# Optimization experiments

Measured on AMD Instinct MI355X. Metric: run time of the kernel, lower is better.

The kernel has to match this reference:

```python
import jax, jax.numpy as jnp
import numpy as np

B, S, D, H = 4, 2048, 1024, 16
HD = D // H          # head_dim = 64; per-head scale = sqrt(HD) as in source
FF = 4096
EPS = 1e-5


def _layernorm(x, g, b):
    m = jnp.mean(x, axis=-1, keepdims=True)
    v = jnp.mean(jnp.square(x - m), axis=-1, keepdims=True)
    return (x - m) * jax.lax.rsqrt(v + EPS) * g + b


def setup_inputs() -> dict:
    key = jax.random.key(0)
    ks = jax.random.split(key, 10)
    std = 0.02
    return {
        "x": jax.random.normal(ks[0], (B, S, D), jnp.float32),
        "wq": jax.random.normal(ks[1], (H, D, HD), jnp.float32) * std,
        "bq": jnp.zeros((H, HD), jnp.float32),
        "wk": jax.random.normal(ks[2], (H, D, HD), jnp.float32) * std,
        "bk": jnp.zeros((H, HD), jnp.float32),
        "wv": jax.random.normal(ks[3], (H, D, HD), jnp.float32) * std,
        "bv": jnp.zeros((H, HD), jnp.float32),
        "wo": jax.random.normal(ks[4], (D, D), jnp.float32) * std,
        "bo": jnp.zeros((D,), jnp.float32),
        "w1": jax.random.normal(ks[5], (D, FF), jnp.float32) * std,
        "b1": jnp.zeros((FF,), jnp.float32),
        "w2": jax.random.normal(ks[6], (FF, D), jnp.float32) * std,
        "b2": jnp.zeros((D,), jnp.float32),
        "g1": jnp.ones((D,), jnp.float32),
        "beta1": jnp.zeros((D,), jnp.float32),
        "g2": jnp.ones((D,), jnp.float32),
        "beta2": jnp.zeros((D,), jnp.float32),
    }


def reference(x, wq, bq, wk, bk, wv, bv, wo, bo, w1, b1, w2, b2, g1, beta1, g2, beta2):
    # Per-head Q/K/V projections (stacked over heads) -> [B,H,S,HD]
    q = jnp.einsum('bsd,hdf->bhsf', x, wq) + bq[None, :, None, :]
    k = jnp.einsum('bsd,hdf->bhsf', x, wk) + bk[None, :, None, :]
    v = jnp.einsum('bsd,hdf->bhsf', x, wv) + bv[None, :, None, :]

    scale = jnp.sqrt(jnp.asarray(HD, jnp.float32))
    att = jnp.einsum('bhqf,bhkf->bhqk', q, k) / scale  # [B,H,S,S]
    causal = jnp.tril(jnp.ones((S, S), dtype=bool))
    att = jnp.where(causal[None, None], att, -jnp.inf)
    p = jax.nn.softmax(att, axis=-1)
    o = jnp.einsum('bhqk,bhkf->bhqf', p, v)            # [B,H,S,HD]
    o = o.transpose(0, 2, 1, 3).reshape(B, S, D)       # concat heads
    attn_out = o @ wo + bo

    h = _layernorm(x + attn_out, g1, beta1)            # post-LN, dropout=0 (eval)
    ff = jax.nn.gelu(h @ w1 + b1, approximate=False) @ w2 + b2
    return _layernorm(h + ff, g2, beta2)
```

## Files before the change

kernel.cpp:

```cpp
#include <hip/hip_runtime.h>
#include <hip/hip_bf16.h>
#include <math.h>

typedef __bf16 bf16x8 __attribute__((ext_vector_type(8)));
typedef float floatx4 __attribute__((ext_vector_type(4)));
typedef unsigned short ushort8 __attribute__((ext_vector_type(8)));
typedef unsigned short ushort4v __attribute__((ext_vector_type(4)));

__device__ __forceinline__ unsigned short f2bs(float f){
  union { float f; unsigned u; } v; v.f = f;
  unsigned r = v.u + 0x7fffu + ((v.u >> 16) & 1u);
  return (unsigned short)(r >> 16);
}
__device__ __forceinline__ float bs2f(unsigned short s){
  union { unsigned u; float f; } v; v.u = ((unsigned)s) << 16; return v.f;
}
__device__ __forceinline__ unsigned pk2(float a, float b){
  union { __hip_bfloat162 h; unsigned u; } cv;
  cv.h = __float22bfloat162_rn(make_float2(a, b));
  return cv.u;
}
__device__ __forceinline__ void gl_lds16(const void* g, void* l){
  __builtin_amdgcn_global_load_lds(
      (const __attribute__((address_space(1))) void*)g,
      (__attribute__((address_space(3))) void*)l,
      16, 0, 0);
}

__global__ __launch_bounds__(256) void cvt_x(const float* __restrict__ x,
                                             unsigned short* __restrict__ o){
  const int i = (blockIdx.x*256 + threadIdx.x)*4;
  const float4 v = *(const float4*)(x + i);
  ushort4v u = { f2bs(v.x), f2bs(v.y), f2bs(v.z), f2bs(v.w) };
  *(ushort4v*)(o + i) = u;
}

__global__ __launch_bounds__(256) void transpose_pack(const float* __restrict__ src,
                                                      unsigned short* __restrict__ dst,
                                                      int R, int C){
  __shared__ float tile[32][65];
  const int r0 = blockIdx.y*32, c0 = blockIdx.x*64;
  const int t = threadIdx.x;
  {
    const int r = t >> 3, cc = (t & 7)*8;
    const float* p = src + (size_t)(r0+r)*C + c0 + cc;
    const float4 v0 = *(const float4*)p;
    const float4 v1 = *(const float4*)(p+4);
    tile[r][cc+0]=v0.x; tile[r][cc+1]=v0.y; tile[r][cc+2]=v0.z; tile[r][cc+3]=v0.w;
    tile[r][cc+4]=v1.x; tile[r][cc+5]=v1.y; tile[r][cc+6]=v1.z; tile[r][cc+7]=v1.w;
  }
  __syncthreads();
  const int f = t >> 2, rr = (t & 3)*8;
  ushort8 u;
  #pragma unroll
  for (int j=0;j<8;j++) u[j] = f2bs(tile[rr+j][f]);
  *(ushort8*)(dst + (size_t)(c0+f)*R + r0 + rr) = u;
}

__global__ __launch_bounds__(256) void pack_qkv(const float* __restrict__ wq,
                                                const float* __restrict__ wk,
                                                const float* __restrict__ wv,
                                                const float* __restrict__ bq,
                                                const float* __restrict__ bk,
                                                const float* __restrict__ bv,
                                                unsigned short* __restrict__ Wt,
                                                float* __restrict__ Bc){
  __shared__ float tile[32][65];
  const int dt = blockIdx.x, h = blockIdx.y, sel = blockIdx.z;
  const float* src = (sel==0 ? wq : (sel==1 ? wk : wv)) + (size_t)h*65536;
  const int t = threadIdx.x, d0 = dt*32;
  {
    const int r = t >> 3, cc = (t & 7)*8;
    const float* p = src + (size_t)(d0+r)*64 + cc;
    const float4 v0 = *(const float4*)p;
    const float4 v1 = *(const float4*)(p+4);
    tile[r][cc+0]=v0.x; tile[r][cc+1]=v0.y; tile[r][cc+2]=v0.z; tile[r][cc+3]=v0.w;
    tile[r][cc+4]=v1.x; tile[r][cc+5]=v1.y; tile[r][cc+6]=v1.z; tile[r][cc+7]=v1.w;
  }
  __syncthreads();
  const int f = t >> 2, rr = (t & 3)*8;
  ushort8 u;
  #pragma unroll
  for (int j=0;j<8;j++) u[j] = f2bs(tile[rr+j][f]);
  const size_t n = (size_t)sel*1024 + h*64 + f;
  *(ushort8*)(Wt + n*1024 + d0 + rr) = u;
  if (dt==0 && t<64){
    const float* bs = (sel==0 ? bq : (sel==1 ? bk : bv)) + h*64;
    Bc[sel*1024 + h*64 + t] = bs[t];
  }
}

template<int MODE>
__global__ __launch_bounds__(256, 4)
void gemm_tn(const unsigned short* __restrict__ A,
             const unsigned short* __restrict__ Bt,
             const float* __restrict__ bias,
             void* __restrict__ out0,
             void* __restrict__ out1,
             void* __restrict__ out2,
             int K, int OW, int klen){
  __shared__ __align__(16) unsigned short As[128*32];
  __shared__ __align__(16) unsigned short Bs[128*32];
  const int tid = threadIdx.x;
  const int wave = tid >> 6, lane = tid & 63;
  const int quad = lane >> 4, l15 = lane & 15;
  const int lin = blockIdx.x;
  const int n0 = (lin & 63) << 7;
  const int m0 = (lin >> 6) << 7;
  const int kz = blockIdx.z;
  const int kbase = kz * klen;
  const int wr = (wave >> 1) << 6, wc = (wave & 1) << 6;

  floatx4 acc[4][4];
  #pragma unroll
  for (int i=0;i<4;i++)
    #pragma unroll
    for (int j=0;j<4;j++) acc[i][j] = (floatx4)0.0f;

  const unsigned short* gA[2];
  const unsigned short* gB[2];
  int lofs[2];
  #pragma unroll
  for (int r2=0;r2<2;r2++){
    const int slot = r2*256 + tid;
    const int rp = slot >> 3, rem = slot & 7;
    const int row = rp*2 + (rem >> 2);
    const int kc = (rem & 3) ^ (rp & 3);
    gA[r2] = A  + (size_t)(m0 + row)*K + kbase + kc*8;
    gB[r2] = Bt + (size_t)(n0 + row)*K + kbase + kc*8;
    lofs[r2] = slot*8;
  }
  int aofs[4], bofs[4];
  #pragma unroll
  for (int t=0;t<4;t++){
    const int ra = wr + t*16 + l15;
    aofs[t] = (ra>>1)*64 + (ra&1)*32 + ((quad ^ ((ra>>1)&3))<<3);
    const int rb = wc + t*16 + l15;
    bofs[t] = (rb>>1)*64 + (rb&1)*32 + ((quad ^ ((rb>>1)&3))<<3);
  }

  for (int k0 = 0; k0 < klen; k0 += 32){
    gl_lds16(gA[0] + k0, As + lofs[0]);
    gl_lds16(gA[1] + k0, As + lofs[1]);
    gl_lds16(gB[0] + k0, Bs + lofs[0]);
    gl_lds16(gB[1] + k0, Bs + lofs[1]);
    __syncthreads();
    bf16x8 af[4];
    #pragma unroll
    for (int t=0;t<4;t++) af[t] = *(const bf16x8*)(&As[aofs[t]]);
    #pragma unroll
    for (int j=0;j<4;j++){
      const bf16x8 bv = *(const bf16x8*)(&Bs[bofs[j]]);
      #pragma unroll
      for (int i=0;i<4;i++)
        acc[i][j] = __builtin_amdgcn_mfma_f32_16x16x32_bf16(af[i], bv, acc[i][j], 0,0,0);
    }
    __syncthreads();
  }

  #pragma unroll
  for (int i=0;i<4;i++){
    const int row0 = m0 + wr + i*16 + quad*4;
    float4 b4 = make_float4(0.f,0.f,0.f,0.f);
    if (MODE != 4 || kz == 0) b4 = *(const float4*)(bias + row0);
    #pragma unroll
    for (int j=0;j<4;j++){
      const int tok = n0 + wc + j*16 + l15;
      float v0 = acc[i][j][0] + b4.x;
      float v1 = acc[i][j][1] + b4.y;
      float v2 = acc[i][j][2] + b4.z;
      float v3 = acc[i][j][3] + b4.w;
      if (MODE == 1){
        float4 o4; o4.x=v0; o4.y=v1; o4.z=v2; o4.w=v3;
        *(float4*)((float*)out0 + (size_t)tok*OW + row0) = o4;
      } else if (MODE == 2){
        float vv[4] = {v0,v1,v2,v3};
        #pragma unroll
        for (int r=0;r<4;r++){
          const float v = vv[r];
          const float u = 0.7978845608f*v*(1.0f + 0.044715f*v*v);
          const float e = __builtin_amdgcn_exp2f(u * 2.885390082f);
          vv[r] = 0.5f*v*(1.0f + (1.0f - 2.0f/(1.0f + e)));
        }
        uint2 pkd = make_uint2(pk2(vv[0], vv[1]), pk2(vv[2], vv[3]));
        *(uint2*)((unsigned short*)out0 + (size_t)tok*4096 + row0) = pkd;
      } else if (MODE == 4){
        uint2 pkd = make_uint2(pk2(v0, v1), pk2(v2, v3));
        unsigned short* o = (unsigned short*)(kz ? out1 : out0);
        *(uint2*)(o + (size_t)tok*1024 + row0) = pkd;
      } else {
        if (row0 < 1024){
          const float s = 0.18033688011112042f;
          uint2 pkd = make_uint2(pk2(v0*s, v1*s), pk2(v2*s, v3*s));
          *(uint2*)((unsigned short*)out0 + (size_t)tok*1024 + row0) = pkd;
        } else if (row0 < 2048){
          uint2 pkd = make_uint2(pk2(v0, v1), pk2(v2, v3));
          *(uint2*)((unsigned short*)out1 + (size_t)tok*1024 + (row0-1024)) = pkd;
        } else {
          uint2 pkd = make_uint2(pk2(v0, v1), pk2(v2, v3));
          *(uint2*)((unsigned short*)out2 + (size_t)tok*1024 + (row0-2048)) = pkd;
        }
      }
    }
  }
}

#define VMCNT4 asm volatile("s_waitcnt vmcnt(4)" ::: "memory")
#define VMCNT0 asm volatile("s_waitcnt vmcnt(0)" ::: "memory")
#define TAILW { if (tg < NT-2) VMCNT4; else VMCNT0; }
#define LGKM4 { asm volatile("s_waitcnt lgkmcnt(4)" ::: "memory"); __builtin_amdgcn_sched_barrier(0); }
#define LGKM8 { asm volatile("s_waitcnt lgkmcnt(8)" ::: "memory"); __builtin_amdgcn_sched_barrier(0); }
#define LGKM0 { asm volatile("s_waitcnt lgkmcnt(0)" ::: "memory"); __builtin_amdgcn_sched_barrier(0); }
#define PHASE_SYNC                                                            \
    __builtin_amdgcn_s_barrier();                                             \
    asm volatile("s_waitcnt lgkmcnt(0)" ::: "memory");                        \
    __builtin_amdgcn_sched_barrier(0);

#define STAGE_A(T, H) { const int T_ = (T); if (T_ < NT){                     \
    unsigned short* l_ = lds + (T_&1)*32768 + (H)*8192;                       \
    const int ko_ = kbase + (T_<<6);                                          \
    gl_lds16(srcA##H##_0 + ko_, l_ + ch0*8);                                  \
    gl_lds16(srcA##H##_1 + ko_, l_ + ch1*8); } }
#define STAGE_B(T, H) { const int T_ = (T); if (T_ < NT){                     \
    unsigned short* l_ = lds + (T_&1)*32768 + 16384 + (H)*8192;               \
    const int ko_ = kbase + (T_<<6);                                          \
    gl_lds16(srcB##H##_0 + ko_, l_ + ch0*8);                                  \
    gl_lds16(srcB##H##_1 + ko_, l_ + ch1*8); } }

#define MFMA_Q(AF, BF, MH, NH)                                                \
    __builtin_amdgcn_s_setprio(1);                                            \
    _Pragma("unroll")                                                         \
    for (int k_=0;k_<2;k_++)                                                  \
      _Pragma("unroll")                                                       \
      for (int m_=0;m_<4;m_++)                                                \
        _Pragma("unroll")                                                     \
        for (int n_=0;n_<2;n_++)                                              \
          acc[(MH)*4+m_][(NH)*2+n_] = __builtin_amdgcn_mfma_f32_16x16x32_bf16( \
              AF[m_][k_], BF[n_][k_], acc[(MH)*4+m_][(NH)*2+n_], 0,0,0);      \
    __builtin_amdgcn_s_setprio(0);

#define RD_A(DST, BASE)                                                       \
    _Pragma("unroll")                                                         \
    for (int m_=0;m_<4;m_++)                                                  \
      _Pragma("unroll")                                                       \
      for (int k_=0;k_<2;k_++) DST[m_][k_] = *(const bf16x8*)((BASE) + aoff[m_][k_]);
#define RD_B(DST, BASE)                                                       \
    _Pragma("unroll")                                                         \
    for (int n_=0;n_<2;n_++)                                                  \
      _Pragma("unroll")                                                       \
      for (int k_=0;k_<2;k_++) DST[n_][k_] = *(const bf16x8*)((BASE) + boff[n_][k_]);

template<int MODE, int PIPE>
__global__ __launch_bounds__(512, 2)
void gemm256(const unsigned short* __restrict__ A,
             const unsigned short* __restrict__ Bt,
             const float* __restrict__ bias,
             void* __restrict__ out0,
             void* __restrict__ out1,
             void* __restrict__ out2,
             int K, int klen){
  __shared__ __align__(16) unsigned short lds[65536];
  const int tid = threadIdx.x;
  const int wave = tid >> 6, lane = tid & 63;
  const int quad = lane >> 4, l15 = lane & 15;
  const int wm = wave >> 2, wn = wave & 3;
  const int lin = blockIdx.x;
  const int n0 = (lin & 31) << 8;
  const int m0 = (lin >> 5) << 8;
  const int kz = blockIdx.z;
  const int kbase = kz * klen;
  const int NT = klen >> 6;

  const int r0 = tid >> 3;
  const int r1 = r0 + 64;
  const int g0 = (tid & 7) ^ (r0 & 7);
  const int ch0 = tid, ch1 = tid + 512;

  const unsigned short* srcA0_0 = A  + (size_t)(m0 +       r0)*K + g0*8;
  const unsigned short* srcA0_1 = A  + (size_t)(m0 +       r1)*K + g0*8;
  const unsigned short* srcA1_0 = A  + (size_t)(m0 + 128 + r0)*K + g0*8;
  const unsigned short* srcA1_1 = A  + (size_t)(m0 + 128 + r1)*K + g0*8;
  const unsigned short* srcB0_0 = Bt + (size_t)(n0 +       r0)*K + g0*8;
  const unsigned short* srcB0_1 = Bt + (size_t)(n0 +       r1)*K + g0*8;
  const unsigned short* srcB1_0 = Bt + (size_t)(n0 + 128 + r0)*K + g0*8;
  const unsigned short* srcB1_1 = Bt + (size_t)(n0 + 128 + r1)*K + g0*8;

  const int xr = l15 & 7;
  int aoff[4][2], boff[2][2];
  #pragma unroll
  for (int m=0;m<4;m++){
    const int rh = wm*64 + m*16 + l15;
    #pragma unroll
    for (int k=0;k<2;k++)
      aoff[m][k] = rh*64 + (((k*4 + quad) ^ xr) << 3);
  }
  #pragma unroll
  for (int n=0;n<2;n++){
    const int rb = wn*32 + n*16 + l15;
    #pragma unroll
    for (int k=0;k<2;k++)
      boff[n][k] = rb*64 + (((k*4 + quad) ^ xr) << 3);
  }

  floatx4 acc[8][4];
  #pragma unroll
  for (int i=0;i<8;i++)
    #pragma unroll
    for (int j=0;j<4;j++) acc[i][j] = (floatx4)0.0f;

  bf16x8 af0[4][2], af1[4][2], bf0[2][2], bf1[2][2];

  STAGE_B(0,0); STAGE_A(0,0); STAGE_A(0,1); STAGE_B(0,1);
  STAGE_B(1,0); STAGE_A(1,0);
  VMCNT4;
  __builtin_amdgcn_s_barrier();

  if (PIPE == 0){
    for (int tg = 0; tg < NT; ++tg){
      const int d = tg & 1;
      const unsigned short* A0b = lds + d*32768;
      const unsigned short* A1b = A0b + 8192;
      const unsigned short* B0b = lds + d*32768 + 16384;
      const unsigned short* B1b = B0b + 8192;

      RD_A(af0, A0b);
      RD_B(bf0, B0b);
      STAGE_A(tg+1, 1);
      PHASE_SYNC;
      MFMA_Q(af0, bf0, 0, 0);
      __builtin_amdgcn_s_barrier();

      RD_B(bf1, B1b);
      STAGE_B(tg+1, 1);
      PHASE_SYNC;
      MFMA_Q(af0, bf1, 0, 1);
      __builtin_amdgcn_s_barrier();

      RD_A(af1, A1b);
      STAGE_B(tg+2, 0);
      PHASE_SYNC;
      MFMA_Q(af1, bf1, 1, 1);
      __builtin_amdgcn_s_barrier();

      STAGE_A(tg+2, 0);
      PHASE_SYNC;
      MFMA_Q(af1, bf0, 1, 0);
      TAILW;
      __builtin_amdgcn_s_barrier();
    }
  } else {
    RD_A(af0, lds);
    RD_B(bf0, lds + 16384);

    for (int tg = 0; tg < NT; ++tg){
      const int d = tg & 1;
      const unsigned short* A1b = lds + d*32768 + 8192;
      const unsigned short* B1b = lds + d*32768 + 16384 + 8192;

      RD_B(bf1, B1b);
      STAGE_A(tg+1, 1);
      LGKM4;
      MFMA_Q(af0, bf0, 0, 0);

      RD_A(af1, A1b);
      STAGE_B(tg+1, 1);
      LGKM8;
      MFMA_Q(af0, bf1, 0, 1);
      __builtin_amdgcn_s_barrier();

      STAGE_B(tg+2, 0);
      LGKM0;
      MFMA_Q(af1, bf1, 1, 1);

      STAGE_A(tg+2, 0);
      TAILW;
      __builtin_amdgcn_s_barrier();
      {
        const unsigned short* A0n = lds + (d^1)*32768;
        const unsigned short* B0n = A0n + 16384;
        if (tg+1 < NT){ RD_A(af0, A0n); }
        MFMA_Q(af1, bf0, 1, 0);
        if (tg+1 < NT){ RD_B(bf0, B0n); }
      }
    }
  }

  #pragma unroll
  for (int mh=0; mh<2; mh++){
    #pragma unroll
    for (int m=0; m<4; m++){
      const int row0 = m0 + mh*128 + wm*64 + m*16 + quad*4;
      float4 b4 = make_float4(0.f,0.f,0.f,0.f);
      if (MODE != 4 || kz == 0) b4 = *(const float4*)(bias + row0);
      #pragma unroll
      for (int nh=0; nh<2; nh++){
        #pragma unroll
        for (int n=0; n<2; n++){
          const int tok = n0 + nh*128 + wn*32 + n*16 + l15;
          const floatx4 a = acc[mh*4+m][nh*2+n];
          float v0 = a[0]+b4.x, v1 = a[1]+b4.y, v2 = a[2]+b4.z, v3 = a[3]+b4.w;
          if (MODE == 2){
            float vv[4] = {v0,v1,v2,v3};
            #pragma unroll
            for (int r=0;r<4;r++){
              const float v = vv[r];
              const float u = 0.7978845608f*v*(1.0f + 0.044715f*v*v);
              const float e = __builtin_amdgcn_exp2f(u * 2.885390082f);
              vv[r] = 0.5f*v*(1.0f + (1.0f - 2.0f/(1.0f + e)));
            }
            uint2 pkd = make_uint2(pk2(vv[0], vv[1]), pk2(vv[2], vv[3]));
            *(uint2*)((unsigned short*)out0 + (size_t)tok*4096 + row0) = pkd;
          } else if (MODE == 4){
            uint2 pkd = make_uint2(pk2(v0, v1), pk2(v2, v3));
            unsigned short* o = (unsigned short*)(kz ? out1 : out0);
            *(uint2*)(o + (size_t)tok*1024 + row0) = pkd;
          } else {
            if (row0 < 1024){
              const float s = 0.18033688011112042f;
              uint2 pkd = make_uint2(pk2(v0*s, v1*s), pk2(v2*s, v3*s));
              *(uint2*)((unsigned short*)out0 + (size_t)tok*1024 + row0) = pkd;
            } else if (row0 < 2048){
              uint2 pkd = make_uint2(pk2(v0, v1), pk2(v2, v3));
              *(uint2*)((unsigned short*)out1 + (size_t)tok*1024 + (row0-1024)) = pkd;
            } else {
              uint2 pkd = make_uint2(pk2(v0, v1), pk2(v2, v3));
              *(uint2*)((unsigned short*)out2 + (size_t)tok*1024 + (row0-2048)) = pkd;
            }
          }
        }
      }
    }
  }
}

__global__ __launch_bounds__(256) void vtrans(const unsigned short* __restrict__ Vtok,
                                              unsigned short* __restrict__ Vt){
  __shared__ unsigned short tile[64][65];
  const int st = blockIdx.x, bh = blockIdx.y;
  const int b = bh >> 4, h = bh & 15;
  const int t = threadIdx.x;
  {
    const int r = t >> 2, cc = (t & 3) * 16;
    const unsigned short* src = Vtok + (size_t)((b<<11) + (st<<6) + r)*1024 + (h<<6) + cc;
    ushort8 u0 = *(const ushort8*)src;
    ushort8 u1 = *(const ushort8*)(src + 8);
    #pragma unroll
    for (int j=0;j<8;j++){ tile[r][cc+j] = u0[j]; tile[r][cc+8+j] = u1[j]; }
  }
  __syncthreads();
  const int f = t >> 2, ss = (t & 3) * 16;
  ushort8 w0, w1;
  #pragma unroll
  for (int j=0;j<8;j++){ w0[j] = tile[ss+j][f]; w1[j] = tile[ss+8+j][f]; }
  unsigned short* dst = Vt + (size_t)bh*64*2048 + (size_t)f*2048 + (st<<6) + ss;
  *(ushort8*)dst = w0;
  *(ushort8*)(dst + 8) = w1;
}

__global__ __launch_bounds__(256, 4) void attn(const unsigned short* __restrict__ Q,
                                               const unsigned short* __restrict__ Kg,
                                               const unsigned short* __restrict__ Vt,
                                               unsigned short* __restrict__ O){
  __shared__ __align__(16) unsigned short Ks[64*64];
  __shared__ __align__(16) unsigned short Vs[64*64];
  __shared__ __align__(16) unsigned short PT[4][2][16*68];

  const int lin = blockIdx.x;
  const int bh = lin & 63;
  const int qt_lo = lin >> 6;
  const int qt_hi = 31 - qt_lo;
  const int b = bh >> 4, h = bh & 15;
  const int tid = threadIdx.x, wave = tid >> 6, lane = tid & 63;
  const int quad = lane >> 4, l15 = lane & 15;
  const float FM = 12.0f;

  const size_t qbase = (size_t)((b<<11) + (wave<<4) + l15)*1024 + (h<<6);
  bf16x8 qf_hi[2], qf_lo[2];
  qf_hi[0] = *(const bf16x8*)(Q + qbase + (size_t)(qt_hi<<6)*1024 + quad*8);
  qf_hi[1] = *(const bf16x8*)(Q + qbase + (size_t)(qt_hi<<6)*1024 + 32 + quad*8);
  qf_lo[0] = *(const bf16x8*)(Q + qbase + (size_t)(qt_lo<<6)*1024 + quad*8);
  qf_lo[1] = *(const bf16x8*)(Q + qbase + (size_t)(qt_lo<<6)*1024 + 32 + quad*8);

  floatx4 oa_hi[4], oa_lo[4];
  #pragma unroll
  for (int i=0;i<4;i++){ oa_hi[i] = (floatx4)0.0f; oa_lo[i] = (floatx4)0.0f; }
  float li_hi = 0.0f, li_lo = 0.0f;

  const unsigned short* Kbh = Kg + ((size_t)(b<<11))*1024 + (h<<6);
  const unsigned short* Vbh = Vt + (size_t)bh*64*2048;
  unsigned short* Pw0 = &PT[wave][0][0];
  unsigned short* Pw1 = &PT[wave][1][0];

  const int slot0 = wave*128 + lane;
  const int krow0 = slot0 >> 3, kc0 = (slot0 & 7) ^ (krow0 & 7);
  const int slot1 = slot0 + 64;
  const int krow1 = slot1 >> 3, kc1 = (slot1 & 7) ^ (krow1 & 7);

  auto softmax_P = [&](floatx4* sa, float& li, unsigned short* Pbuf, bool diag){
    if (diag){
      const int qrow = (wave<<4) + l15;
      #pragma unroll
      for (int tj=0;tj<4;tj++)
        #pragma unroll
        for (int r=0;r<4;r++)
          if (tj*16 + quad*4 + r > qrow) sa[tj][r] = -1e30f;
    }
    float rs = 0.0f;
    #pragma unroll
    for (int tj=0;tj<4;tj++)
      #pragma unroll
      for (int r=0;r<4;r++){
        const float p = __builtin_amdgcn_exp2f(sa[tj][r] - FM);
        sa[tj][r] = p;
        rs += p;
      }
    li += rs;
    #pragma unroll
    for (int tj=0;tj<4;tj++){
      uint2 pkd = make_uint2(pk2(sa[tj][0], sa[tj][1]), pk2(sa[tj][2], sa[tj][3]));
      *(uint2*)(Pbuf + l15*68 + tj*16 + quad*4) = pkd;
    }
  };

  for (int kt = 0; kt <= qt_hi; ++kt){
    gl_lds16(Kbh + (size_t)((kt<<6) + krow0)*1024 + kc0*8, Ks + wave*1024);
    gl_lds16(Kbh + (size_t)((kt<<6) + krow1)*1024 + kc1*8, Ks + wave*1024 + 512);
    gl_lds16(Vbh + (size_t)krow0*2048 + (kt<<6) + kc0*8, Vs + wave*1024);
    gl_lds16(Vbh + (size_t)krow1*2048 + (kt<<6) + kc1*8, Vs + wave*1024 + 512);
    __syncthreads();

    if (kt <= qt_lo){
      floatx4 sh[4], sl[4];
      __builtin_amdgcn_s_setprio(1);
      #pragma unroll
      for (int tj=0;tj<4;tj++){
        sh[tj] = (floatx4)0.0f; sl[tj] = (floatx4)0.0f;
        #pragma unroll
        for (int ks=0;ks<2;ks++){
          const int n = tj*16 + l15;
          const int c = (ks*4 + quad) ^ (n & 7);
          const bf16x8 kf = *(const bf16x8*)(Ks + n*64 + c*8);
          sh[tj] = __builtin_amdgcn_mfma_f32_16x16x32_bf16(kf, qf_hi[ks], sh[tj], 0,0,0);
          sl[tj] = __builtin_amdgcn_mfma_f32_16x16x32_bf16(kf, qf_lo[ks], sl[tj], 0,0,0);
        }
      }
      __builtin_amdgcn_s_setprio(0);
      softmax_P(sh, li_hi, Pw0, false);
      softmax_P(sl, li_lo, Pw1, kt == qt_lo);
      __builtin_amdgcn_s_setprio(1);
      #pragma unroll
      for (int ks2=0;ks2<2;ks2++){
        const bf16x8 pfh = *(const bf16x8*)(Pw0 + l15*68 + ks2*32 + quad*8);
        const bf16x8 pfl = *(const bf16x8*)(Pw1 + l15*68 + ks2*32 + quad*8);
        #pragma unroll
        for (int tn=0;tn<4;tn++){
          const int n2 = tn*16 + l15;
          const int c = (ks2*4 + quad) ^ (n2 & 7);
          const bf16x8 vf = *(const bf16x8*)(Vs + n2*64 + c*8);
          oa_hi[tn] = __builtin_amdgcn_mfma_f32_16x16x32_bf16(vf, pfh, oa_hi[tn], 0,0,0);
          oa_lo[tn] = __builtin_amdgcn_mfma_f32_16x16x32_bf16(vf, pfl, oa_lo[tn], 0,0,0);
        }
      }
      __builtin_amdgcn_s_setprio(0);
    } else {
      floatx4 sh[4];
      __builtin_amdgcn_s_setprio(1);
      #pragma unroll
      for (int tj=0;tj<4;tj++){
        sh[tj] = (floatx4)0.0f;
        #pragma unroll
        for (int ks=0;ks<2;ks++){
          const int n = tj*16 + l15;
          const int c = (ks*4 + quad) ^ (n & 7);
          const bf16x8 kf = *(const bf16x8*)(Ks + n*64 + c*8);
          sh[tj] = __builtin_amdgcn_mfma_f32_16x16x32_bf16(kf, qf_hi[ks], sh[tj], 0,0,0);
        }
      }
      __builtin_amdgcn_s_setprio(0);
      softmax_P(sh, li_hi, Pw0, kt == qt_hi);
      __builtin_amdgcn_s_setprio(1);
      #pragma unroll
      for (int ks2=0;ks2<2;ks2++){
        const bf16x8 pfh = *(const bf16x8*)(Pw0 + l15*68 + ks2*32 + quad*8);
        #pragma unroll
        for (int tn=0;tn<4;tn++){
          const int n2 = tn*16 + l15;
          const int c = (ks2*4 + quad) ^ (n2 & 7);
          const bf16x8 vf = *(const bf16x8*)(Vs + n2*64 + c*8);
          oa_hi[tn] = __builtin_amdgcn_mfma_f32_16x16x32_bf16(vf, pfh, oa_hi[tn], 0,0,0);
        }
      }
      __builtin_amdgcn_s_setprio(0);
    }
    __syncthreads();
  }

  li_hi += __shfl_xor(li_hi, 16, 64);
  li_hi += __shfl_xor(li_hi, 32, 64);
  li_lo += __shfl_xor(li_lo, 16, 64);
  li_lo += __shfl_xor(li_lo, 32, 64);
  {
    const float inv = 1.0f / li_hi;
    unsigned short* Orow = O + (size_t)((b<<11) + (qt_hi<<6) + (wave<<4) + l15)*1024 + (h<<6);
    #pragma unroll
    for (int tn=0;tn<4;tn++){
      uint2 pkd = make_uint2(pk2(oa_hi[tn][0]*inv, oa_hi[tn][1]*inv),
                             pk2(oa_hi[tn][2]*inv, oa_hi[tn][3]*inv));
      *(uint2*)(Orow + tn*16 + quad*4) = pkd;
    }
  }
  {
    const float inv = 1.0f / li_lo;
    unsigned short* Orow = O + (size_t)((b<<11) + (qt_lo<<6) + (wave<<4) + l15)*1024 + (h<<6);
    #pragma unroll
    for (int tn=0;tn<4;tn++){
      uint2 pkd = make_uint2(pk2(oa_lo[tn][0]*inv, oa_lo[tn][1]*inv),
                             pk2(oa_lo[tn][2]*inv, oa_lo[tn][3]*inv));
      *(uint2*)(Orow + tn*16 + quad*4) = pkd;
    }
  }
}

__global__ __launch_bounds__(256) void ln_res(const float* __restrict__ a,
                                              const float* __restrict__ bsrc,
                                              const float* __restrict__ g,
                                              const float* __restrict__ be,
                                              float* __restrict__ of,
                                              unsigned short* __restrict__ ob){
  __shared__ float red1[4], red2[4];
  const int row = blockIdx.x, t = threadIdx.x;
  const int wave = t >> 6, lane = t & 63;
  const float4 va = *(const float4*)(a + (size_t)row*1024 + t*4);
  const float4 vb = *(const float4*)(bsrc + (size_t)row*1024 + t*4);
  float xs[4] = {va.x+vb.x, va.y+vb.y, va.z+vb.z, va.w+vb.w};
  float s = xs[0]+xs[1]+xs[2]+xs[3];
  #pragma unroll
  for (int d=1; d<64; d<<=1) s += __shfl_xor(s, d, 64);
  if (lane==0) red1[wave] = s;
  __syncthreads();
  const float mean = (red1[0]+red1[1]+red1[2]+red1[3]) * (1.0f/1024.0f);
  float vsum = 0.0f;
  #pragma unroll
  for (int i=0;i<4;i++){ const float d = xs[i]-mean; vsum += d*d; }
  #pragma unroll
  for (int d=1; d<64; d<<=1) vsum += __shfl_xor(vsum, d, 64);
  if (lane==0) red2[wave] = vsum;
  __syncthreads();
  const float var = (red2[0]+red2[1]+red2[2]+red2[3]) * (1.0f/1024.0f);
  const float rs = rsqrtf(var + 1e-5f);
  const float4 gg = *(const float4*)(g + t*4);
  const float4 bb = *(const float4*)(be + t*4);
  float y[4];
  y[0] = (xs[0]-mean)*rs*gg.x + bb.x;
  y[1] = (xs[1]-mean)*rs*gg.y + bb.y;
  y[2] = (xs[2]-mean)*rs*gg.z + bb.z;
  y[3] = (xs[3]-mean)*rs*gg.w + bb.w;
  if (of){
    float4 o4; o4.x=y[0]; o4.y=y[1]; o4.z=y[2]; o4.w=y[3];
    *(float4*)(of + (size_t)row*1024 + t*4) = o4;
  }
  if (ob){
    ushort4v u = { f2bs(y[0]), f2bs(y[1]), f2bs(y[2]), f2bs(y[3]) };
    *(ushort4v*)(ob + (size_t)row*1024 + t*4) = u;
  }
}

__global__ __launch_bounds__(256) void ln_res2(const float* __restrict__ a,
                                               const unsigned short* __restrict__ p0,
                                               const unsigned short* __restrict__ p1,
                                               const float* __restrict__ g,
                                               const float* __restrict__ be,
                                               float* __restrict__ of){
  __shared__ float red1[4], red2[4];
  const int row = blockIdx.x, t = threadIdx.x;
  const int wave = t >> 6, lane = t & 63;
  const float4 va = *(const float4*)(a + (size_t)row*1024 + t*4);
  const ushort4v u0 = *(const ushort4v*)(p0 + (size_t)row*1024 + t*4);
  const ushort4v u1 = *(const ushort4v*)(p1 + (size_t)row*1024 + t*4);
  float xs[4] = { va.x + bs2f(u0[0]) + bs2f(u1[0]),
                  va.y + bs2f(u0[1]) + bs2f(u1[1]),
                  va.z + bs2f(u0[2]) + bs2f(u1[2]),
                  va.w + bs2f(u0[3]) + bs2f(u1[3]) };
  float s = xs[0]+xs[1]+xs[2]+xs[3];
  #pragma unroll
  for (int d=1; d<64; d<<=1) s += __shfl_xor(s, d, 64);
  if (lane==0) red1[wave] = s;
  __syncthreads();
  const float mean = (red1[0]+red1[1]+red1[2]+red1[3]) * (1.0f/1024.0f);
  float vsum = 0.0f;
  #pragma unroll
  for (int i=0;i<4;i++){ const float d = xs[i]-mean; vsum += d*d; }
  #pragma unroll
  for (int d=1; d<64; d<<=1) vsum += __shfl_xor(vsum, d, 64);
  if (lane==0) red2[wave] = vsum;
  __syncthreads();
  const float var = (red2[0]+red2[1]+red2[2]+red2[3]) * (1.0f/1024.0f);
  const float rs = rsqrtf(var + 1e-5f);
  const float4 gg = *(const float4*)(g + t*4);
  const float4 bb = *(const float4*)(be + t*4);
  float4 o4;
  o4.x = (xs[0]-mean)*rs*gg.x + bb.x;
  o4.y = (xs[1]-mean)*rs*gg.y + bb.y;
  o4.z = (xs[2]-mean)*rs*gg.z + bb.z;
  o4.w = (xs[3]-mean)*rs*gg.w + bb.w;
  *(float4*)(of + (size_t)row*1024 + t*4) = o4;
}

extern "C" void kernel_launch(void* const* d_in, const int* in_sizes, int n_in,
                              void* d_out, int out_size, void* d_ws, size_t ws_size,
                              hipStream_t stream){
  (void)in_sizes; (void)n_in; (void)out_size; (void)ws_size;
  const float* x  = (const float*)d_in[0];
  const float* wq = (const float*)d_in[1];
  const float* bq = (const float*)d_in[2];
  const float* wk = (const float*)d_in[3];
  const float* bk = (const float*)d_in[4];
  const float* wv = (const float*)d_in[5];
  const float* bv = (const float*)d_in[6];
  const float* wo = (const float*)d_in[7];
  const float* bo = (const float*)d_in[8];
  const float* w1 = (const float*)d_in[9];
  const float* b1 = (const float*)d_in[10];
  const float* w2 = (const float*)d_in[11];
  const float* b2 = (const float*)d_in[12];
  const float* g1 = (const float*)d_in[13];
  const float* be1= (const float*)d_in[14];
  const float* g2 = (const float*)d_in[15];
  const float* be2= (const float*)d_in[16];
  float* out = (float*)d_out;

  char* ws = (char*)d_ws;
  size_t off = 0;
  auto take = [&](size_t bytes)->char*{
    char* p = ws + off; off += (bytes + 255) & ~(size_t)255; return p;
  };
  unsigned short* Xb  = (unsigned short*)take(8192UL*1024*2);
  unsigned short* Qb  = (unsigned short*)take(8192UL*1024*2);
  unsigned short* Kb  = (unsigned short*)take(8192UL*1024*2);
  unsigned short* Vtb = (unsigned short*)take(8192UL*1024*2);
  unsigned short* Ob  = (unsigned short*)take(8192UL*1024*2);
  unsigned short* Midb= Qb;
  unsigned short* Vtok= (unsigned short*)take(8192UL*1024*2);
  unsigned short* Wqkv= (unsigned short*)take(3072UL*1024*2);
  float*          Bqkv= (float*)take(3072UL*4);
  unsigned short* Wot = (unsigned short*)take(1024UL*1024*2);
  unsigned short* W1t = (unsigned short*)take(4096UL*1024*2);
  unsigned short* W2t = (unsigned short*)take(1024UL*4096*2);
  float*          C1  = (float*)take(8192UL*1024*4);
  unsigned short* F0  = (unsigned short*)C1;
  unsigned short* F1  = F0 + 8192UL*1024;
  float*          Hf  = (float*)take(8192UL*1024*4);
  unsigned short* Hb  = (unsigned short*)take(8192UL*1024*2);

  cvt_x<<<8192, 256, 0, stream>>>(x, Xb);
  pack_qkv<<<dim3(32,16,3), 256, 0, stream>>>(wq, wk, wv, bq, bk, bv, Wqkv, Bqkv);
  transpose_pack<<<dim3(16,32),  256, 0, stream>>>(wo, Wot, 1024, 1024);
  transpose_pack<<<dim3(64,32),  256, 0, stream>>>(w1, W1t, 1024, 4096);
  transpose_pack<<<dim3(16,128), 256, 0, stream>>>(w2, W2t, 4096, 1024);

  gemm256<3,1><<<12*32, 512, 0, stream>>>(Wqkv, Xb, Bqkv, Qb, Kb, Vtok, 1024, 1024);
  vtrans<<<dim3(32,64), 256, 0, stream>>>(Vtok, Vtb);

  attn<<<1024, 256, 0, stream>>>(Qb, Kb, Vtb, Ob);

  gemm_tn<1><<<8*64, 256, 0, stream>>>(Wot, Ob, bo, C1, nullptr, nullptr, 1024, 1024, 1024);
  ln_res<<<8192, 256, 0, stream>>>(x, C1, g1, be1, Hf, Hb);

  gemm256<2,0><<<16*32, 512, 0, stream>>>(W1t, Hb, b1, Midb, nullptr, nullptr, 1024, 1024);
  gemm256<4,1><<<dim3(4*32,1,2), 512, 0, stream>>>(W2t, Midb, b2, F0, F1, nullptr, 4096, 2048);
  ln_res2<<<8192, 256, 0, stream>>>(Hf, F0, F1, g2, be2, out);
}
```

Before: 505.0 us.

## Fuse prep kernels into one launch and register-prefetch K/V tiles in attention

```diff
diff --git a/kernel.cpp b/kernel.cpp
--- a/kernel.cpp
+++ b/kernel.cpp
@@ -27,20 +27,58 @@
       16, 0, 0);
 }
 
-__global__ __launch_bounds__(256) void cvt_x(const float* __restrict__ x,
-                                             unsigned short* __restrict__ o){
-  const int i = (blockIdx.x*256 + threadIdx.x)*4;
-  const float4 v = *(const float4*)(x + i);
-  ushort4v u = { f2bs(v.x), f2bs(v.y), f2bs(v.z), f2bs(v.w) };
-  *(ushort4v*)(o + i) = u;
-}
-
-__global__ __launch_bounds__(256) void transpose_pack(const float* __restrict__ src,
-                                                      unsigned short* __restrict__ dst,
-                                                      int R, int C){
+__global__ __launch_bounds__(256) void prep(
+    const float* __restrict__ x,  unsigned short* __restrict__ Xb,
+    const float* __restrict__ wq, const float* __restrict__ wk,
+    const float* __restrict__ wv, const float* __restrict__ bq,
+    const float* __restrict__ bk, const float* __restrict__ bv,
+    unsigned short* __restrict__ Wqkv, float* __restrict__ Bqkv,
+    const float* __restrict__ wo, unsigned short* __restrict__ Wot,
+    const float* __restrict__ w1, unsigned short* __restrict__ W1t,
+    const float* __restrict__ w2, unsigned short* __restrict__ W2t){
   __shared__ float tile[32][65];
-  const int r0 = blockIdx.y*32, c0 = blockIdx.x*64;
-  const int t = threadIdx.x;
+  const int blk = blockIdx.x, t = threadIdx.x;
+
+  if (blk < 8192){
+    const int i = (blk*256 + t)*4;
+    const float4 v = *(const float4*)(x + i);
+    ushort4v u = { f2bs(v.x), f2bs(v.y), f2bs(v.z), f2bs(v.w) };
+    *(ushort4v*)(Xb + i) = u;
+    return;
+  }
+
+  if (blk < 9728){
+    const int p = blk - 8192;
+    const int dt = p & 31, h = (p>>5)&15, sel = p>>9;
+    const float* src = (sel==0 ? wq : (sel==1 ? wk : wv)) + (size_t)h*65536;
+    const int d0 = dt*32;
+    {
+      const int r = t >> 3, cc = (t & 7)*8;
+      const float* pp = src + (size_t)(d0+r)*64 + cc;
+      const float4 v0 = *(const float4*)pp;
+      const float4 v1 = *(const float4*)(pp+4);
+      tile[r][cc+0]=v0.x; tile[r][cc+1]=v0.y; tile[r][cc+2]=v0.z; tile[r][cc+3]=v0.w;
+      tile[r][cc+4]=v1.x; tile[r][cc+5]=v1.y; tile[r][cc+6]=v1.z; tile[r][cc+7]=v1.w;
+    }
+    __syncthreads();
+    const int f = t >> 2, rr = (t & 3)*8;
+    ushort8 u;
+    #pragma unroll
+    for (int j=0;j<8;j++) u[j] = f2bs(tile[rr+j][f]);
+    const size_t n = (size_t)sel*1024 + h*64 + f;
+    *(ushort8*)(Wqkv + n*1024 + d0 + rr) = u;
+    if (dt==0 && t<64){
+      const float* bs = (sel==0 ? bq : (sel==1 ? bk : bv)) + h*64;
+      Bqkv[sel*1024 + h*64 + t] = bs[t];
+    }
+    return;
+  }
+
+  const float* src; unsigned short* dst; int R, C, bx, by;
+  if (blk < 10240){ const int q = blk-9728;  src=wo; dst=Wot; R=1024; C=1024; bx=q&15; by=q>>4; }
+  else if (blk < 12288){ const int q = blk-10240; src=w1; dst=W1t; R=1024; C=4096; bx=q&63; by=q>>6; }
+  else { const int q = blk-12288; src=w2; dst=W2t; R=4096; C=1024; bx=q&15; by=q>>4; }
+  const int r0 = by*32, c0 = bx*64;
   {
     const int r = t >> 3, cc = (t & 7)*8;
     const float* p = src + (size_t)(r0+r)*C + c0 + cc;
@@ -55,39 +93,6 @@
   #pragma unroll
   for (int j=0;j<8;j++) u[j] = f2bs(tile[rr+j][f]);
   *(ushort8*)(dst + (size_t)(c0+f)*R + r0 + rr) = u;
-}
-
-__global__ __launch_bounds__(256) void pack_qkv(const float* __restrict__ wq,
-                                                const float* __restrict__ wk,
-                                                const float* __restrict__ wv,
-                                                const float* __restrict__ bq,
-                                                const float* __restrict__ bk,
-                                                const float* __restrict__ bv,
-                                                unsigned short* __restrict__ Wt,
-                                                float* __restrict__ Bc){
-  __shared__ float tile[32][65];
-  const int dt = blockIdx.x, h = blockIdx.y, sel = blockIdx.z;
-  const float* src = (sel==0 ? wq : (sel==1 ? wk : wv)) + (size_t)h*65536;
-  const int t = threadIdx.x, d0 = dt*32;
-  {
-    const int r = t >> 3, cc = (t & 7)*8;
-    const float* p = src + (size_t)(d0+r)*64 + cc;
-    const float4 v0 = *(const float4*)p;
-    const float4 v1 = *(const float4*)(p+4);
-    tile[r][cc+0]=v0.x; tile[r][cc+1]=v0.y; tile[r][cc+2]=v0.z; tile[r][cc+3]=v0.w;
-    tile[r][cc+4]=v1.x; tile[r][cc+5]=v1.y; tile[r][cc+6]=v1.z; tile[r][cc+7]=v1.w;
-  }
-  __syncthreads();
-  const int f = t >> 2, rr = (t & 3)*8;
-  ushort8 u;
-  #pragma unroll
-  for (int j=0;j<8;j++) u[j] = f2bs(tile[rr+j][f]);
-  const size_t n = (size_t)sel*1024 + h*64 + f;
-  *(ushort8*)(Wt + n*1024 + d0 + rr) = u;
-  if (dt==0 && t<64){
-    const float* bs = (sel==0 ? bq : (sel==1 ? bk : bv)) + h*64;
-    Bc[sel*1024 + h*64 + t] = bs[t];
-  }
 }
 
 template<int MODE>
@@ -496,6 +501,20 @@
   const int slot1 = slot0 + 64;
   const int krow1 = slot1 >> 3, kc1 = (slot1 & 7) ^ (krow1 & 7);
 
+  ushort8 kr0, kr1, vr0, vr1;
+  auto load_kv = [&](int kt){
+    kr0 = *(const ushort8*)(Kbh + (size_t)((kt<<6) + krow0)*1024 + kc0*8);
+    kr1 = *(const ushort8*)(Kbh + (size_t)((kt<<6) + krow1)*1024 + kc1*8);
+    vr0 = *(const ushort8*)(Vbh + (size_t)krow0*2048 + (kt<<6) + kc0*8);
+    vr1 = *(const ushort8*)(Vbh + (size_t)krow1*2048 + (kt<<6) + kc1*8);
+  };
+  auto write_kv = [&](){
+    *(ushort8*)(Ks + wave*1024 + lane*8)       = kr0;
+    *(ushort8*)(Ks + wave*1024 + 512 + lane*8) = kr1;
+    *(ushort8*)(Vs + wave*1024 + lane*8)       = vr0;
+    *(ushort8*)(Vs + wave*1024 + 512 + lane*8) = vr1;
+  };
+
   auto softmax_P = [&](floatx4* sa, float& li, unsigned short* Pbuf, bool diag){
     if (diag){
       const int qrow = (wave<<4) + l15;
@@ -522,12 +541,11 @@
     }
   };
 
+  load_kv(0); write_kv();
+  __syncthreads();
+
   for (int kt = 0; kt <= qt_hi; ++kt){
-    gl_lds16(Kbh + (size_t)((kt<<6) + krow0)*1024 + kc0*8, Ks + wave*1024);
-    gl_lds16(Kbh + (size_t)((kt<<6) + krow1)*1024 + kc1*8, Ks + wave*1024 + 512);
-    gl_lds16(Vbh + (size_t)krow0*2048 + (kt<<6) + kc0*8, Vs + wave*1024);
-    gl_lds16(Vbh + (size_t)krow1*2048 + (kt<<6) + kc1*8, Vs + wave*1024 + 512);
-    __syncthreads();
+    if (kt < qt_hi) load_kv(kt+1);
 
     if (kt <= qt_lo){
       floatx4 sh[4], sl[4];
@@ -592,6 +610,9 @@
       }
       __builtin_amdgcn_s_setprio(0);
     }
+
+    __syncthreads();
+    if (kt < qt_hi) write_kv();
     __syncthreads();
   }
 
@@ -752,11 +773,8 @@
   float*          Hf  = (float*)take(8192UL*1024*4);
   unsigned short* Hb  = (unsigned short*)take(8192UL*1024*2);
 
-  cvt_x<<<8192, 256, 0, stream>>>(x, Xb);
-  pack_qkv<<<dim3(32,16,3), 256, 0, stream>>>(wq, wk, wv, bq, bk, bv, Wqkv, Bqkv);
-  transpose_pack<<<dim3(16,32),  256, 0, stream>>>(wo, Wot, 1024, 1024);
-  transpose_pack<<<dim3(64,32),  256, 0, stream>>>(w1, W1t, 1024, 4096);
-  transpose_pack<<<dim3(16,128), 256, 0, stream>>>(w2, W2t, 4096, 1024);
+  prep<<<14336, 256, 0, stream>>>(x, Xb, wq, wk, wv, bq, bk, bv,
+                                  Wqkv, Bqkv, wo, Wot, w1, W1t, w2, W2t);
 
   gemm256<3,1><<<12*32, 512, 0, stream>>>(Wqkv, Xb, Bqkv, Qb, Kb, Vtok, 1024, 1024);
   vtrans<<<dim3(32,64), 256, 0, stream>>>(Vtok, Vtb);
```

Result: slower. 561.8 us (+11.3%).
